# Kernel tuning notes

Hardware: AMD Instinct MI355X
Metric: run time of the kernel (lower is better)

## Reference

```python
import jax, jax.numpy as jnp
import numpy as np

N = 65536      # nodes
E = 524288     # edges (avg degree 8)
C = 128        # in_channels == hidden_channels
L = 3          # num_layers
EPS = 1e-5     # BatchNorm eps


def setup_inputs() -> dict:
    key = jax.random.key(0)
    ks = jax.random.split(key, 12)
    inv = 1.0 / np.sqrt(C)
    return {
        "x": jax.random.normal(ks[0], (N, C), jnp.float32),
        "edge_weight": jax.random.uniform(ks[1], (E,), jnp.float32),
        "bn_gamma": 1.0 + 0.1 * jax.random.normal(ks[2], (L, C), jnp.float32),
        "bn_beta": 0.1 * jax.random.normal(ks[3], (L, C), jnp.float32),
        "W_self": inv * jax.random.normal(ks[4], (L, C, C), jnp.float32),
        "W_neigh": inv * jax.random.normal(ks[5], (L, C, C), jnp.float32),
        "bias": 0.01 * jax.random.normal(ks[6], (L, C), jnp.float32),
        "lin_w": inv * jax.random.normal(ks[7], (C,), jnp.float32),
        "lin_b": 0.01 * jax.random.normal(ks[8], (), jnp.float32),
        "src": jax.random.randint(ks[9], (E,), 0, N),
        "dst": jax.random.randint(ks[10], (E,), 0, N),
    }


def reference(x, edge_weight, bn_gamma, bn_beta, W_self, W_neigh, bias, lin_w, lin_b, src, dst):
    # log1p on edge weights (done once in the torch module per layer; identical each layer)
    ew = jnp.log1p(edge_weight)[:, None]                     # [E,1]
    # in-degree for mean aggregation (DGL fn.mean); isolated nodes -> divide by 1 (sum is 0)
    deg = jax.ops.segment_sum(jnp.ones((E,), x.dtype), dst, num_segments=N)
    deg = jnp.maximum(deg, 1.0)[:, None]                     # [N,1]

    h = x
    for l in range(L):
        # BatchNorm1d over nodes (training-mode batch stats, biased variance)
        mu = jnp.mean(h, axis=0)
        var = jnp.mean((h - mu) ** 2, axis=0)
        h = (h - mu) * jax.lax.rsqrt(var + EPS) * bn_gamma[l] + bn_beta[l]
        # SAGEConv mean aggregator: msg = h[src] * w, neigh = mean over in-edges
        msg = h[src] * ew                                    # [E,C]
        neigh = jax.ops.segment_sum(msg, dst, num_segments=N) / deg  # [N,C]
        h = jax.nn.relu(h @ W_self[l] + neigh @ W_neigh[l] + bias[l])
    return h @ lin_w + lin_b                                 # [N]
```

## Files before the change

kernel.cpp:

```cpp
#include <hip/hip_runtime.h>
#include <hip/hip_fp16.h>

#define NN 65536
#define EE 524288
#define CC 128
#define CAP 40

typedef _Float16 f16x8 __attribute__((ext_vector_type(8)));
typedef float f32x4 __attribute__((ext_vector_type(4)));


__global__ void k_convert(const float* __restrict__ x, __half* __restrict__ h,
                          float* __restrict__ pstat0) {
    int t = threadIdx.x, b = blockIdx.x;
    const float4* xv = (const float4*)x;
    __half2* o = (__half2*)h;
    float s[4] = {0, 0, 0, 0}, q[4] = {0, 0, 0, 0};
    for (int k = 0; k < 32; k++) {
        int i = b * 8192 + k * 256 + t;
        float4 v = xv[i];
        o[2 * i]     = __floats2half2_rn(v.x, v.y);
        o[2 * i + 1] = __floats2half2_rn(v.z, v.w);
        s[0] += v.x; s[1] += v.y; s[2] += v.z; s[3] += v.w;
        q[0] += v.x * v.x; q[1] += v.y * v.y; q[2] += v.z * v.z; q[3] += v.w * v.w;
    }
    __shared__ float ls[256];
    ls[t] = 0.f;
    __syncthreads();
    int c0 = (t & 31) * 4;
#pragma unroll
    for (int u = 0; u < 4; u++) {
        atomicAdd(&ls[c0 + u], s[u]);
        atomicAdd(&ls[128 + c0 + u], q[u]);
    }
    __syncthreads();
    if (t < 128) {
        atomicAdd(&pstat0[t], ls[t]);
        atomicAdd(&pstat0[128 + t], ls[128 + t]);
    }
}

__global__ void k_scatter(const int* __restrict__ src, const int* __restrict__ dst,
                          const float* __restrict__ ew,
                          int* __restrict__ cnt, unsigned int* __restrict__ buf) {
    int e = blockIdx.x * blockDim.x + threadIdx.x;
    int d = dst[e];
    int pos = atomicAdd(&cnt[d], 1);
    float w = log1pf(ew[e]);
    unsigned int pk = (unsigned int)src[e] |
                      ((unsigned int)__half_as_ushort(__float2half(w)) << 16);
    if (pos < CAP) buf[d * CAP + pos] = pk;
}


__global__ void k_fold(const float* __restrict__ pstat_l,
                       const float* __restrict__ gamma, const float* __restrict__ beta,
                       const float* __restrict__ Ws, const float* __restrict__ Wn,
                       const float* __restrict__ bias,
                       __half* __restrict__ Wcat, float* __restrict__ crow,
                       float* __restrict__ cneigh) {
    int c = blockIdx.x, k = threadIdx.x;
    float mu = pstat_l[k] * (1.0f / NN);
    float var = pstat_l[128 + k] * (1.0f / NN) - mu * mu;
    float alpha = rsqrtf(var + 1e-5f) * gamma[k];
    float delta = beta[k] - mu * alpha;
    float ws = Ws[k * 128 + c];
    float wn = Wn[k * 128 + c];
    Wcat[c * 256 + k]       = __float2half(alpha * ws);
    Wcat[c * 256 + 128 + k] = __float2half(alpha * wn);
    float rs = delta * ws, rn = delta * wn;
#pragma unroll
    for (int off = 1; off < 64; off <<= 1) {
        rs += __shfl_xor(rs, off);
        rn += __shfl_xor(rn, off);
    }
    __shared__ float tmp[4];
    if ((k & 63) == 0) { tmp[(k >> 6) * 2] = rs; tmp[(k >> 6) * 2 + 1] = rn; }
    __syncthreads();
    if (k == 0) {
        crow[c]   = bias[c] + tmp[0] + tmp[2];
        cneigh[c] = tmp[1] + tmp[3];
    }
}

__global__ void k_agg(const __half2* __restrict__ h, const int* __restrict__ cnt,
                      const unsigned int* __restrict__ buf,
                      __half2* __restrict__ aggn, float* __restrict__ sod, int writeSod) {
    int lane = threadIdx.x & 63;
    int n = blockIdx.x * 4 + (threadIdx.x >> 6);
    int d = cnt[n];
    if (d > CAP) d = CAP;
    unsigned int pk = 0;
    if (lane < d) pk = buf[n * CAP + lane];
    float ax0 = 0, ay0 = 0, ax1 = 0, ay1 = 0;
    float ax2 = 0, ay2 = 0, ax3 = 0, ay3 = 0;
    int j = 0;
    for (; j + 4 <= d; j += 4) {
        unsigned int p0 = __shfl(pk, j),     p1 = __shfl(pk, j + 1);
        unsigned int p2 = __shfl(pk, j + 2), p3 = __shfl(pk, j + 3);
        float2 v0 = __half22float2(h[(p0 & 0xFFFF) * 64 + lane]);
        float2 v1 = __half22float2(h[(p1 & 0xFFFF) * 64 + lane]);
        float2 v2 = __half22float2(h[(p2 & 0xFFFF) * 64 + lane]);
        float2 v3 = __half22float2(h[(p3 & 0xFFFF) * 64 + lane]);
        float w0 = __half2float(__ushort_as_half((unsigned short)(p0 >> 16)));
        float w1 = __half2float(__ushort_as_half((unsigned short)(p1 >> 16)));
        float w2 = __half2float(__ushort_as_half((unsigned short)(p2 >> 16)));
        float w3 = __half2float(__ushort_as_half((unsigned short)(p3 >> 16)));
        ax0 += w0 * v0.x; ay0 += w0 * v0.y;
        ax1 += w1 * v1.x; ay1 += w1 * v1.y;
        ax2 += w2 * v2.x; ay2 += w2 * v2.y;
        ax3 += w3 * v3.x; ay3 += w3 * v3.y;
    }
    for (; j < d; j++) {
        unsigned int p0 = __shfl(pk, j);
        float2 v0 = __half22float2(h[(p0 & 0xFFFF) * 64 + lane]);
        float w0 = __half2float(__ushort_as_half((unsigned short)(p0 >> 16)));
        ax0 += w0 * v0.x; ay0 += w0 * v0.y;
    }
    float ax = (ax0 + ax1) + (ax2 + ax3);
    float ay = (ay0 + ay1) + (ay2 + ay3);
    float inv = 1.0f / (float)(d > 1 ? d : 1);
    aggn[n * 64 + lane] = __floats2half2_rn(ax * inv, ay * inv);
    if (writeSod) {
        float wsum = (lane < d) ? __half2float(__ushort_as_half((unsigned short)(pk >> 16))) : 0.f;
#pragma unroll
        for (int off = 1; off < 64; off <<= 1) wsum += __shfl_xor(wsum, off);
        if (lane == 0) sod[n] = wsum * inv;
    }
}

__launch_bounds__(256, 2)
__global__ void k_gemm(const __half* hA, const __half* __restrict__ aggn,
                       const __half* __restrict__ Wcat,
                       const float* __restrict__ crow, const float* __restrict__ cneigh,
                       const float* __restrict__ sod,
                       const float* __restrict__ lin_w, const float* __restrict__ lin_b,
                       __half* hout, float* __restrict__ outv, int mode,
                       float* __restrict__ pstatN) {
    __shared__ __half Bl[128 * 136];
    int tid = threadIdx.x;
    int lane = tid & 63;
    int wvid = tid >> 6;
    int l15 = lane & 15, quad = lane >> 4;
    int i0 = blockIdx.x * 128;

    f32x4 acc0[8], acc1[8];
    f32x4 zero = {0.f, 0.f, 0.f, 0.f};
#pragma unroll
    for (int t = 0; t < 8; t++) { acc0[t] = zero; acc1[t] = zero; }

#pragma unroll
    for (int chunk = 0; chunk < 2; chunk++) {
        const __half* Asrc = chunk ? aggn : hA;
        f16x8 af0[4], af1[4];
#pragma unroll
        for (int s = 0; s < 4; s++) {
            int kof = s * 32 + quad * 8;
            af0[s] = *(const f16x8*)&Asrc[(i0 + wvid * 32 + l15) * 128 + kof];
            af1[s] = *(const f16x8*)&Asrc[(i0 + wvid * 32 + 16 + l15) * 128 + kof];
        }
        __syncthreads();
#pragma unroll
        for (int it = 0; it < 8; it++) {
            int m = tid * 8 + it * 2048;
            int c = m >> 7, kl = m & 127;
            *(f16x8*)&Bl[c * 136 + kl] = *(const f16x8*)&Wcat[c * 256 + chunk * 128 + kl];
        }
        __syncthreads();
#pragma unroll
        for (int s = 0; s < 4; s++) {
#pragma unroll
            for (int tn = 0; tn < 8; tn++) {
                f16x8 bf = *(const f16x8*)&Bl[(tn * 16 + l15) * 136 + s * 32 + quad * 8];
                acc0[tn] = __builtin_amdgcn_mfma_f32_16x16x32_f16(af0[s], bf, acc0[tn], 0, 0, 0);
                acc1[tn] = __builtin_amdgcn_mfma_f32_16x16x32_f16(af1[s], bf, acc1[tn], 0, 0, 0);
            }
        }
    }

    float cr[8], cn[8];
#pragma unroll
    for (int tn = 0; tn < 8; tn++) {
        cr[tn] = crow[tn * 16 + l15];
        cn[tn] = cneigh[tn * 16 + l15];
    }
    int rwbase = i0 + wvid * 32 + quad * 4;

    if (mode == 0) {
        float cs[8], cq[8];
#pragma unroll
        for (int tn = 0; tn < 8; tn++) { cs[tn] = 0.f; cq[tn] = 0.f; }
#pragma unroll
        for (int tm = 0; tm < 2; tm++) {
#pragma unroll
            for (int r = 0; r < 4; r++) {
                int row = rwbase + tm * 16 + r;
                float sdv = sod[row];
#pragma unroll
                for (int tn = 0; tn < 8; tn++) {
                    float v = (tm ? acc1[tn][r] : acc0[tn][r]) + cr[tn] + sdv * cn[tn];
                    v = fmaxf(v, 0.f);
                    hout[row * 128 + tn * 16 + l15] = __float2half(v);
                    cs[tn] += v;
                    cq[tn] += v * v;
                }
            }
        }
#pragma unroll
        for (int tn = 0; tn < 8; tn++) {
            cs[tn] += __shfl_xor(cs[tn], 16); cs[tn] += __shfl_xor(cs[tn], 32);
            cq[tn] += __shfl_xor(cq[tn], 16); cq[tn] += __shfl_xor(cq[tn], 32);
        }
        __syncthreads();
        float* st = (float*)Bl;
        st[tid] = 0.f;
        __syncthreads();
        if (lane < 16) {
#pragma unroll
            for (int tn = 0; tn < 8; tn++) {
                atomicAdd(&st[tn * 16 + l15], cs[tn]);
                atomicAdd(&st[128 + tn * 16 + l15], cq[tn]);
            }
        }
        __syncthreads();
        if (tid < 128) {
            atomicAdd(&pstatN[tid], st[tid]);
            atomicAdd(&pstatN[128 + tid], st[128 + tid]);
        }
    } else {
        float lw[8];
#pragma unroll
        for (int tn = 0; tn < 8; tn++) lw[tn] = lin_w[tn * 16 + l15];
        float lb = lin_b[0];
#pragma unroll
        for (int tm = 0; tm < 2; tm++) {
#pragma unroll
            for (int r = 0; r < 4; r++) {
                int row = rwbase + tm * 16 + r;
                float sdv = sod[row];
                float p = 0.f;
#pragma unroll
                for (int tn = 0; tn < 8; tn++) {
                    float v = (tm ? acc1[tn][r] : acc0[tn][r]) + cr[tn] + sdv * cn[tn];
                    v = fmaxf(v, 0.f);
                    p += v * lw[tn];
                }
                p += __shfl_xor(p, 1);
                p += __shfl_xor(p, 2);
                p += __shfl_xor(p, 4);
                p += __shfl_xor(p, 8);
                if (l15 == 0) outv[row] = p + lb;
            }
        }
    }
}


extern "C" void kernel_launch(void* const* d_in, const int* in_sizes, int n_in,
                              void* d_out, int out_size, void* d_ws, size_t ws_size,
                              hipStream_t stream) {
    (void)in_sizes; (void)n_in; (void)out_size; (void)ws_size;
    const float* x     = (const float*)d_in[0];
    const float* ew    = (const float*)d_in[1];
    const float* gamma = (const float*)d_in[2];
    const float* beta  = (const float*)d_in[3];
    const float* Ws    = (const float*)d_in[4];
    const float* Wn    = (const float*)d_in[5];
    const float* bias  = (const float*)d_in[6];
    const float* lin_w = (const float*)d_in[7];
    const float* lin_b = (const float*)d_in[8];
    const int*   srcI  = (const int*)d_in[9];
    const int*   dstI  = (const int*)d_in[10];
    float* out = (float*)d_out;

    char* p = (char*)d_ws;
    __half* h    = (__half*)p; p += (size_t)NN * CC * 2;
    __half* aggn = (__half*)p; p += (size_t)NN * CC * 2;
    __half* Wcat = (__half*)p; p += 256 * 128 * 2;
    float* crow   = (float*)p; p += 512;
    float* cneigh = (float*)p; p += 512;
    float* sod    = (float*)p; p += (size_t)NN * 4;
    unsigned int* buf = (unsigned int*)p; p += (size_t)NN * CAP * 4;
    int*   cnt    = (int*)p;   p += (size_t)NN * 4;
    float* pstat  = (float*)p; p += 3 * 256 * 4;

    hipMemsetAsync(cnt, 0, (size_t)NN * 4 + 3 * 256 * 4, stream);

    k_convert<<<dim3(256), dim3(256), 0, stream>>>(x, h, pstat);
    k_scatter<<<dim3(EE / 256), dim3(256), 0, stream>>>(srcI, dstI, ew, cnt, buf);

    for (int l = 0; l < 3; l++) {
        k_fold<<<dim3(128), dim3(128), 0, stream>>>(pstat + l * 256, gamma + l * CC, beta + l * CC,
                                                    Ws + (size_t)l * CC * CC, Wn + (size_t)l * CC * CC,
                                                    bias + l * CC, Wcat, crow, cneigh);
        k_agg<<<dim3(NN / 4), dim3(256), 0, stream>>>((const __half2*)h, cnt, buf,
                                                      (__half2*)aggn, sod, (l == 0) ? 1 : 0);
        int mode = (l == 2) ? 1 : 0;
        float* pstatN = (mode == 0) ? (pstat + (l + 1) * 256) : pstat;
        k_gemm<<<dim3(NN / 128), dim3(256), 0, stream>>>(h, aggn, Wcat, crow, cneigh, sod,
                                                         lin_w, lin_b, h, out, mode, pstatN);
    }
}
```

Baseline: 298.3 us.

## Merge independent kernels via block-range dispatch and widen gather unroll to eight

Fuses the convert and edge-scatter kernels into one launch, and the per-layer BN-fold kernel into the aggregation kernel as extra blocks, so the launch count drops from 11 to 7. The aggregation loop now issues eight independent gathers per round instead of four, with eight accumulator pairs, to keep more memory loads in flight. Rounds are padded to a multiple of eight, and the padding lanes carry pk=0, so they load node 0 with weight zero. That adds wasted gathers for low-degree nodes and raises register use.

```diff
diff --git a/kernel.cpp b/kernel.cpp
--- a/kernel.cpp
+++ b/kernel.cpp
@@ -10,117 +10,119 @@
 typedef float f32x4 __attribute__((ext_vector_type(4)));
 
 
-__global__ void k_convert(const float* __restrict__ x, __half* __restrict__ h,
-                          float* __restrict__ pstat0) {
-    int t = threadIdx.x, b = blockIdx.x;
-    const float4* xv = (const float4*)x;
-    __half2* o = (__half2*)h;
-    float s[4] = {0, 0, 0, 0}, q[4] = {0, 0, 0, 0};
-    for (int k = 0; k < 32; k++) {
-        int i = b * 8192 + k * 256 + t;
-        float4 v = xv[i];
-        o[2 * i]     = __floats2half2_rn(v.x, v.y);
-        o[2 * i + 1] = __floats2half2_rn(v.z, v.w);
-        s[0] += v.x; s[1] += v.y; s[2] += v.z; s[3] += v.w;
-        q[0] += v.x * v.x; q[1] += v.y * v.y; q[2] += v.z * v.z; q[3] += v.w * v.w;
-    }
-    __shared__ float ls[256];
-    ls[t] = 0.f;
-    __syncthreads();
-    int c0 = (t & 31) * 4;
-#pragma unroll
-    for (int u = 0; u < 4; u++) {
-        atomicAdd(&ls[c0 + u], s[u]);
-        atomicAdd(&ls[128 + c0 + u], q[u]);
-    }
-    __syncthreads();
-    if (t < 128) {
-        atomicAdd(&pstat0[t], ls[t]);
-        atomicAdd(&pstat0[128 + t], ls[128 + t]);
+__global__ void k_init(const float* __restrict__ x, __half* __restrict__ h,
+                       float* __restrict__ pstat0,
+                       const int* __restrict__ src, const int* __restrict__ dst,
+                       const float* __restrict__ ew,
+                       int* __restrict__ cnt, unsigned int* __restrict__ buf) {
+    int b = blockIdx.x, t = threadIdx.x;
+    if (b < 256) {
+        const float4* xv = (const float4*)x;
+        __half2* o = (__half2*)h;
+        float s[4] = {0, 0, 0, 0}, q[4] = {0, 0, 0, 0};
+        for (int k = 0; k < 32; k++) {
+            int i = b * 8192 + k * 256 + t;
+            float4 v = xv[i];
+            o[2 * i]     = __floats2half2_rn(v.x, v.y);
+            o[2 * i + 1] = __floats2half2_rn(v.z, v.w);
+            s[0] += v.x; s[1] += v.y; s[2] += v.z; s[3] += v.w;
+            q[0] += v.x * v.x; q[1] += v.y * v.y; q[2] += v.z * v.z; q[3] += v.w * v.w;
+        }
+        __shared__ float ls[256];
+        ls[t] = 0.f;
+        __syncthreads();
+        int c0 = (t & 31) * 4;
+#pragma unroll
+        for (int u = 0; u < 4; u++) {
+            atomicAdd(&ls[c0 + u], s[u]);
+            atomicAdd(&ls[128 + c0 + u], q[u]);
+        }
+        __syncthreads();
+        if (t < 128) {
+            atomicAdd(&pstat0[t], ls[t]);
+            atomicAdd(&pstat0[128 + t], ls[128 + t]);
+        }
+    } else {
+        int e = (b - 256) * 256 + t;
+        int d = dst[e];
+        int pos = atomicAdd(&cnt[d], 1);
+        float w = log1pf(ew[e]);
+        unsigned int pk = (unsigned int)src[e] |
+                          ((unsigned int)__half_as_ushort(__float2half(w)) << 16);
+        if (pos < CAP) buf[d * CAP + pos] = pk;
     }
 }
 
-__global__ void k_scatter(const int* __restrict__ src, const int* __restrict__ dst,
-                          const float* __restrict__ ew,
-                          int* __restrict__ cnt, unsigned int* __restrict__ buf) {
-    int e = blockIdx.x * blockDim.x + threadIdx.x;
-    int d = dst[e];
-    int pos = atomicAdd(&cnt[d], 1);
-    float w = log1pf(ew[e]);
-    unsigned int pk = (unsigned int)src[e] |
-                      ((unsigned int)__half_as_ushort(__float2half(w)) << 16);
-    if (pos < CAP) buf[d * CAP + pos] = pk;
-}
-
-
-__global__ void k_fold(const float* __restrict__ pstat_l,
-                       const float* __restrict__ gamma, const float* __restrict__ beta,
-                       const float* __restrict__ Ws, const float* __restrict__ Wn,
-                       const float* __restrict__ bias,
-                       __half* __restrict__ Wcat, float* __restrict__ crow,
-                       float* __restrict__ cneigh) {
-    int c = blockIdx.x, k = threadIdx.x;
-    float mu = pstat_l[k] * (1.0f / NN);
-    float var = pstat_l[128 + k] * (1.0f / NN) - mu * mu;
-    float alpha = rsqrtf(var + 1e-5f) * gamma[k];
-    float delta = beta[k] - mu * alpha;
-    float ws = Ws[k * 128 + c];
-    float wn = Wn[k * 128 + c];
-    Wcat[c * 256 + k]       = __float2half(alpha * ws);
-    Wcat[c * 256 + 128 + k] = __float2half(alpha * wn);
-    float rs = delta * ws, rn = delta * wn;
-#pragma unroll
-    for (int off = 1; off < 64; off <<= 1) {
-        rs += __shfl_xor(rs, off);
-        rn += __shfl_xor(rn, off);
-    }
-    __shared__ float tmp[4];
-    if ((k & 63) == 0) { tmp[(k >> 6) * 2] = rs; tmp[(k >> 6) * 2 + 1] = rn; }
-    __syncthreads();
-    if (k == 0) {
-        crow[c]   = bias[c] + tmp[0] + tmp[2];
-        cneigh[c] = tmp[1] + tmp[3];
-    }
-}
-
-__global__ void k_agg(const __half2* __restrict__ h, const int* __restrict__ cnt,
-                      const unsigned int* __restrict__ buf,
-                      __half2* __restrict__ aggn, float* __restrict__ sod, int writeSod) {
-    int lane = threadIdx.x & 63;
-    int n = blockIdx.x * 4 + (threadIdx.x >> 6);
+
+__global__ void k_aggfold(const __half2* __restrict__ h, const int* __restrict__ cnt,
+                          const unsigned int* __restrict__ buf,
+                          __half2* __restrict__ aggn, float* __restrict__ sod, int writeSod,
+                          const float* __restrict__ pstat_l,
+                          const float* __restrict__ gamma, const float* __restrict__ beta,
+                          const float* __restrict__ Ws, const float* __restrict__ Wn,
+                          const float* __restrict__ bias,
+                          __half* __restrict__ Wcat, float* __restrict__ crow,
+                          float* __restrict__ cneigh) {
+    int bid = blockIdx.x;
+    int tid = threadIdx.x;
+    if (bid >= NN / 4) {
+        int c = (bid - NN / 4) * 2 + (tid >> 7);
+        int k = tid & 127;
+        float mu = pstat_l[k] * (1.0f / NN);
+        float var = pstat_l[128 + k] * (1.0f / NN) - mu * mu;
+        float alpha = rsqrtf(var + 1e-5f) * gamma[k];
+        float delta = beta[k] - mu * alpha;
+        float ws = Ws[k * 128 + c];
+        float wn = Wn[k * 128 + c];
+        Wcat[c * 256 + k]       = __float2half(alpha * ws);
+        Wcat[c * 256 + 128 + k] = __float2half(alpha * wn);
+        float rs = delta * ws, rn = delta * wn;
+#pragma unroll
+        for (int off = 1; off < 64; off <<= 1) {
+            rs += __shfl_xor(rs, off);
+            rn += __shfl_xor(rn, off);
+        }
+        __shared__ float tmp[8];
+        int wv = tid >> 6;
+        if ((tid & 63) == 0) { tmp[wv * 2] = rs; tmp[wv * 2 + 1] = rn; }
+        __syncthreads();
+        if ((tid & 127) == 0) {
+            int base = (tid >> 7) * 4;
+            crow[c]   = bias[c] + tmp[base + 0] + tmp[base + 2];
+            cneigh[c] = tmp[base + 1] + tmp[base + 3];
+        }
+        return;
+    }
+    int lane = tid & 63;
+    int n = bid * 4 + (tid >> 6);
     int d = cnt[n];
     if (d > CAP) d = CAP;
     unsigned int pk = 0;
     if (lane < d) pk = buf[n * CAP + lane];
-    float ax0 = 0, ay0 = 0, ax1 = 0, ay1 = 0;
-    float ax2 = 0, ay2 = 0, ax3 = 0, ay3 = 0;
-    int j = 0;
-    for (; j + 4 <= d; j += 4) {
-        unsigned int p0 = __shfl(pk, j),     p1 = __shfl(pk, j + 1);
-        unsigned int p2 = __shfl(pk, j + 2), p3 = __shfl(pk, j + 3);
-        float2 v0 = __half22float2(h[(p0 & 0xFFFF) * 64 + lane]);
-        float2 v1 = __half22float2(h[(p1 & 0xFFFF) * 64 + lane]);
-        float2 v2 = __half22float2(h[(p2 & 0xFFFF) * 64 + lane]);
-        float2 v3 = __half22float2(h[(p3 & 0xFFFF) * 64 + lane]);
-        float w0 = __half2float(__ushort_as_half((unsigned short)(p0 >> 16)));
-        float w1 = __half2float(__ushort_as_half((unsigned short)(p1 >> 16)));
-        float w2 = __half2float(__ushort_as_half((unsigned short)(p2 >> 16)));
-        float w3 = __half2float(__ushort_as_half((unsigned short)(p3 >> 16)));
-        ax0 += w0 * v0.x; ay0 += w0 * v0.y;
-        ax1 += w1 * v1.x; ay1 += w1 * v1.y;
-        ax2 += w2 * v2.x; ay2 += w2 * v2.y;
-        ax3 += w3 * v3.x; ay3 += w3 * v3.y;
-    }
-    for (; j < d; j++) {
-        unsigned int p0 = __shfl(pk, j);
-        float2 v0 = __half22float2(h[(p0 & 0xFFFF) * 64 + lane]);
-        float w0 = __half2float(__ushort_as_half((unsigned short)(p0 >> 16)));
-        ax0 += w0 * v0.x; ay0 += w0 * v0.y;
-    }
-    float ax = (ax0 + ax1) + (ax2 + ax3);
-    float ay = (ay0 + ay1) + (ay2 + ay3);
+    float ax[8], ay[8];
+#pragma unroll
+    for (int u = 0; u < 8; u++) { ax[u] = 0.f; ay[u] = 0.f; }
+    int rounds = (d + 7) >> 3;
+    for (int r = 0; r < rounds; r++) {
+        int j = r * 8;
+        unsigned int p[8];
+        __half2 hv[8];
+#pragma unroll
+        for (int u = 0; u < 8; u++) p[u] = __shfl(pk, j + u);
+#pragma unroll
+        for (int u = 0; u < 8; u++) hv[u] = h[(p[u] & 0xFFFF) * 64 + lane];
+#pragma unroll
+        for (int u = 0; u < 8; u++) {
+            float w = __half2float(__ushort_as_half((unsigned short)(p[u] >> 16)));
+            float2 v = __half22float2(hv[u]);
+            ax[u] += w * v.x;
+            ay[u] += w * v.y;
+        }
+    }
+    float axs = ((ax[0] + ax[1]) + (ax[2] + ax[3])) + ((ax[4] + ax[5]) + (ax[6] + ax[7]));
+    float ays = ((ay[0] + ay[1]) + (ay[2] + ay[3])) + ((ay[4] + ay[5]) + (ay[6] + ay[7]));
     float inv = 1.0f / (float)(d > 1 ? d : 1);
-    aggn[n * 64 + lane] = __floats2half2_rn(ax * inv, ay * inv);
+    aggn[n * 64 + lane] = __floats2half2_rn(axs * inv, ays * inv);
     if (writeSod) {
         float wsum = (lane < d) ? __half2float(__ushort_as_half((unsigned short)(pk >> 16))) : 0.f;
 #pragma unroll
@@ -286,15 +288,14 @@
 
     hipMemsetAsync(cnt, 0, (size_t)NN * 4 + 3 * 256 * 4, stream);
 
-    k_convert<<<dim3(256), dim3(256), 0, stream>>>(x, h, pstat);
-    k_scatter<<<dim3(EE / 256), dim3(256), 0, stream>>>(srcI, dstI, ew, cnt, buf);
+    k_init<<<dim3(256 + EE / 256), dim3(256), 0, stream>>>(x, h, pstat, srcI, dstI, ew, cnt, buf);
 
     for (int l = 0; l < 3; l++) {
-        k_fold<<<dim3(128), dim3(128), 0, stream>>>(pstat + l * 256, gamma + l * CC, beta + l * CC,
-                                                    Ws + (size_t)l * CC * CC, Wn + (size_t)l * CC * CC,
-                                                    bias + l * CC, Wcat, crow, cneigh);
-        k_agg<<<dim3(NN / 4), dim3(256), 0, stream>>>((const __half2*)h, cnt, buf,
-                                                      (__half2*)aggn, sod, (l == 0) ? 1 : 0);
+        k_aggfold<<<dim3(NN / 4 + 64), dim3(256), 0, stream>>>(
+            (const __half2*)h, cnt, buf, (__half2*)aggn, sod, (l == 0) ? 1 : 0,
+            pstat + l * 256, gamma + l * CC, beta + l * CC,
+            Ws + (size_t)l * CC * CC, Wn + (size_t)l * CC * CC, bias + l * CC,
+            Wcat, crow, cneigh);
         int mode = (l == 2) ? 1 : 0;
         float* pstatN = (mode == 0) ? (pstat + (l + 1) * 256) : pstat;
         k_gemm<<<dim3(NN / 128), dim3(256), 0, stream>>>(h, aggn, Wcat, crow, cneigh, sod,
```

Result: faster. 268.4 us (-10.0%).
